# Optimization experiments

Hardware: AMD Instinct MI355X
Metric: run time of the kernel (lower is better)

The kernel has to match this reference:

```python
import jax, jax.numpy as jnp
import numpy as np

B, T, G, M, D = 8, 2048, 2, 1024, 256
ALPHA = -1.0      # config['dist_to_logits_alpha']
TAU = 2.0         # curr_temp = max_temp at init
EPS = 1e-10


def setup_inputs() -> dict:
    key = jax.random.key(0)
    k1, k2, k3 = jax.random.split(key, 3)
    x = jax.random.normal(k1, (B, T, G * D), dtype=jnp.float32)
    # nn.init.uniform_(embedding, -0.999, 0.999)
    embedding = jax.random.uniform(k2, (G, M, D), dtype=jnp.float32, minval=-0.999, maxval=0.999)
    # uniform noise for gumbel sampling, clipped away from {0,1}
    gumbel_u = jax.random.uniform(k3, (B * T, G, M), dtype=jnp.float32, minval=1e-6, maxval=1.0 - 1e-6)
    return {"x": x, "embedding": embedding, "gumbel_u": gumbel_u}


def reference(x, embedding, gumbel_u):
    b, t, c = x.shape
    g, m, d = embedding.shape
    xf = x.reshape(-1, g, d)                                  # [N, G, D]

    sq_e = jnp.sum(embedding ** 2, axis=-1)                   # [G, M]
    sq_x = jnp.sum(xf ** 2, axis=-1, keepdims=True)           # [N, G, 1]
    cross = jnp.einsum('ngd,gmd->ngm', xf, embedding)         # [N, G, M]
    logits = ALPHA * (sq_e[None] + sq_x - 2.0 * cross)        # [N, G, M]

    # hard-assignment code perplexity
    hard_x = jax.nn.one_hot(jnp.argmax(logits, axis=-1), m, dtype=logits.dtype)
    hard_probs = hard_x.mean(axis=0)                          # [G, M]
    code_perplexity = -jnp.sum(hard_probs * jnp.log2(hard_probs + EPS), axis=-1)

    # soft-assignment prob perplexity
    avg_probs = jax.nn.softmax(logits, axis=-1).mean(axis=0)  # [G, M]
    prob_perplexity = -jnp.sum(avg_probs * jnp.log2(avg_probs + EPS), axis=-1)

    # gumbel-softmax (hard=True, straight-through)
    gumbels = -jnp.log(-jnp.log(gumbel_u))
    y_soft = jax.nn.softmax((logits + gumbels) / TAU, axis=-1)
    idx = jnp.argmax(y_soft, axis=-1)                         # [N, G]
    y_hard = jax.nn.one_hot(idx, m, dtype=y_soft.dtype)
    st = y_hard + y_soft - jax.lax.stop_gradient(y_soft)      # straight-through one-hot

    # weighted sum over the codebook (avoids [N, G, M, D] blowup of the original)
    quantized = jnp.einsum('ngm,gmd->ngd', st, embedding).reshape(b, t, c)

    quantization_inds = idx.reshape(b, t, g).astype(jnp.int32)
    # use_vq_loss=True: F.mse_loss(x, quantized.detach())
    commitment_loss = jnp.mean((x - jax.lax.stop_gradient(quantized)) ** 2)

    return quantized, code_perplexity, prob_perplexity, quantization_inds, commitment_loss
```

## Files before the change

### kernel.cpp

```cpp
#include <hip/hip_runtime.h>
#include <math.h>

#define NTOT 16384
#define GG 2
#define MM 1024
#define DD 256

#define OFF_Q  ((size_t)0)
#define OFF_CP ((size_t)8388608)
#define OFF_PP ((size_t)8388610)
#define OFF_I  ((size_t)8388612)
#define OFF_L  ((size_t)8421380)

#define SHIFT 40.0f
#define REFINE_GAP 0.03f

typedef __attribute__((ext_vector_type(8))) short bf16x8;
typedef __attribute__((ext_vector_type(4))) float f32x4;
typedef unsigned short u16;
typedef unsigned int u32;

__device__ inline float wave_sum_f(float v) {
#pragma unroll
  for (int o = 32; o > 0; o >>= 1) v += __shfl_xor(v, o);
  return v;
}
__device__ inline u16 f2bf(float f) {
  u32 u = __float_as_uint(f);
  return (u16)((u + 0x7fffu + ((u >> 16) & 1u)) >> 16);
}
__device__ inline float bf2f(u16 h) {
  return __uint_as_float(((u32)h) << 16);
}
__device__ inline void async16(const void* g, void* l) {
  __builtin_amdgcn_global_load_lds(
      (const __attribute__((address_space(1))) u32*)g,
      (__attribute__((address_space(3))) u32*)l, 16, 0, 0);
}

#define WS_INVZ   32768
#define WS_EHSW   163840
#define WS_ELSW   1212416
#define WS_EST    2260992
#define WS_NEED3  (2260992ull + 2ull * MM * (size_t)NTOT * GG)

__global__ void vq_init2(const float* __restrict__ emb, float* __restrict__ sq_e,
                         float* __restrict__ avg, int* __restrict__ hist,
                         double* __restrict__ loss, u16* __restrict__ eh,
                         u16* __restrict__ el, int do_split) {
  const int row = blockIdx.x * 4 + (threadIdx.x >> 6);
  const int lane = threadIdx.x & 63;
  float4 e4 = *(const float4*)&emb[(size_t)row * DD + lane * 4];
  float s = e4.x * e4.x + e4.y * e4.y + e4.z * e4.z + e4.w * e4.w;
  s = wave_sum_f(s);
  if (do_split) {
    ushort4 h, l;
    h.x = f2bf(e4.x); l.x = f2bf(e4.x - bf2f(h.x));
    h.y = f2bf(e4.y); l.y = f2bf(e4.y - bf2f(h.y));
    h.z = f2bf(e4.z); l.z = f2bf(e4.z - bf2f(h.z));
    h.w = f2bf(e4.w); l.w = f2bf(e4.w - bf2f(h.w));
    *(ushort4*)&eh[(size_t)row * DD + lane * 4] = h;
    *(ushort4*)&el[(size_t)row * DD + lane * 4] = l;
  }
  if (lane == 0) sq_e[row] = s;
  if (blockIdx.x == 0) {
    for (int i = threadIdx.x; i < GG * MM; i += 256) { avg[i] = 0.f; hist[i] = 0; }
    if (threadIdx.x == 0) *loss = 0.0;
  }
}

__global__ void vq_init_swz(const float* __restrict__ emb, u16* __restrict__ eh_sw,
                            u16* __restrict__ el_sw) {
  int tid = blockIdx.x * 256 + threadIdx.x;
  int g = tid >> 15, rem = tid & 32767;
  int col = rem >> 5, kc = rem & 31;
  const float* src = emb + ((size_t)(g * MM + col)) * DD + kc * 8;
  float4 fa = *(const float4*)src;
  float4 fb = *(const float4*)(src + 4);
  float f[8] = {fa.x, fa.y, fa.z, fa.w, fb.x, fb.y, fb.z, fb.w};
  u16 hi[8], lo[8];
#pragma unroll
  for (int j = 0; j < 8; ++j) {
    hi[j] = f2bf(f[j]);
    lo[j] = f2bf(f[j] - bf2f(hi[j]));
  }
  int ct = col >> 6, cg = (col >> 4) & 3, l15 = col & 15;
  int ks = kc >> 2, quad = kc & 3;
  size_t chunk = ((((size_t)g * 16 + ct) * 8 + ks) * 4 + cg) * 64 + quad * 16 + l15;
  ushort4* dh = (ushort4*)(eh_sw + chunk * 8);
  ushort4* dl = (ushort4*)(el_sw + chunk * 8);
  dh[0] = make_ushort4(hi[0], hi[1], hi[2], hi[3]);
  dh[1] = make_ushort4(hi[4], hi[5], hi[6], hi[7]);
  dl[0] = make_ushort4(lo[0], lo[1], lo[2], lo[3]);
  dl[1] = make_ushort4(lo[4], lo[5], lo[6], lo[7]);
}

__global__ __launch_bounds__(256, 2) void vq_main3(
    const float* __restrict__ x, const float* __restrict__ emb,
    const float* __restrict__ gum, const float* __restrict__ sq_e,
    const u16* __restrict__ eh_sw, const u16* __restrict__ el_sw,
    float* __restrict__ out, u16* __restrict__ est, float* __restrict__ invZ_ws,
    int* __restrict__ hist, double* __restrict__ loss) {
  __shared__ u16 bt[2][32768];
  __shared__ int fidx_lds[128];

  const int g = blockIdx.y;
  const int n0 = blockIdx.x * 128;
  const int t = threadIdx.x;
  const int wave = t >> 6, lane = t & 63;
  const int quad = lane >> 4, l15 = lane & 15;
  const int nw = n0 + wave * 32;

  float* xs = (float*)&bt[0][0];
  {
    const float* xb = x + (size_t)nw * (GG * DD) + (size_t)g * DD;
#pragma unroll 4
    for (int j = 0; j < 32; ++j) {
      float4 v = *(const float4*)(xb + (size_t)j * (GG * DD) + lane * 4);
      *(float4*)&xs[wave * 8192 + j * 256 + ((lane ^ (j & 7)) << 2)] = v;
    }
  }
  __syncthreads();

  bf16x8 ah[2][8], al[2][8];
#pragma unroll
  for (int s = 0; s < 2; ++s) {
#pragma unroll
    for (int ks = 0; ks < 8; ++ks) {
      int row = s * 16 + l15;
      int c0 = ks * 8 + quad * 2;
      const float* base = &xs[wave * 8192 + row * 256];
      float4 f0 = *(const float4*)&base[((c0 ^ (row & 7)) << 2)];
      float4 f1 = *(const float4*)&base[(((c0 + 1) ^ (row & 7)) << 2)];
      float f[8] = {f0.x, f0.y, f0.z, f0.w, f1.x, f1.y, f1.z, f1.w};
#pragma unroll
      for (int j = 0; j < 8; ++j) {
        u16 h = f2bf(f[j]);
        ah[s][ks][j] = (short)h;
        al[s][ks][j] = (short)f2bf(f[j] - bf2f(h));
      }
    }
  }
  __syncthreads();

  const u16* sgh = eh_sw + (size_t)g * 16 * 16384;
  const u16* sgl = el_sw + (size_t)g * 16 * 16384;

  auto stage = [&](int ct, int buf) {
    const u16* sh = sgh + (size_t)ct * 16384;
    const u16* sl = sgl + (size_t)ct * 16384;
    u16* dh = &bt[buf][0];
    u16* dl = &bt[buf][16384];
#pragma unroll
    for (int j = 0; j < 8; ++j) {
      int slot = j * 4 + wave;
      async16(sh + slot * 512 + lane * 8, dh + slot * 512);
      async16(sl + slot * 512 + lane * 8, dl + slot * 512);
    }
  };

  float Zl[8], hv[8], z1[8], z2[8];
  int hid[8], i1[8], i2[8];
#pragma unroll
  for (int i = 0; i < 8; ++i) {
    Zl[i] = 0.f; hv[i] = -INFINITY; z1[i] = -INFINITY; z2[i] = -INFINITY;
    hid[i] = 0; i1[i] = 0; i2[i] = 0;
  }

  stage(0, 0);

#pragma unroll 1
  for (int ct = 0; ct < 16; ++ct) {
    __syncthreads();
    if (ct < 15) stage(ct + 1, (ct + 1) & 1);
    const u16* bh_p = &bt[ct & 1][0];
    const u16* bl_p = &bt[ct & 1][16384];
#pragma unroll 1
    for (int cg = 0; cg < 4; ++cg) {
      const int colG = ct * 64 + cg * 16 + l15;
      float sqv = sq_e[g * MM + colG];
      float gv[8];
#pragma unroll
      for (int s = 0; s < 2; ++s)
#pragma unroll
        for (int r = 0; r < 4; ++r)
          gv[s * 4 + r] =
              gum[((size_t)(nw + s * 16 + quad * 4 + r) * GG + g) * MM + colG];

      f32x4 c00 = {0,0,0,0}, c01 = {0,0,0,0}, c02 = {0,0,0,0};
      f32x4 c10 = {0,0,0,0}, c11 = {0,0,0,0}, c12 = {0,0,0,0};
#pragma unroll
      for (int ks = 0; ks < 8; ++ks) {
        int off = ((ks * 4 + cg) * 64 + lane) * 8;
        bf16x8 bh = *(const bf16x8*)(bh_p + off);
        bf16x8 bl = *(const bf16x8*)(bl_p + off);
        c00 = __builtin_amdgcn_mfma_f32_16x16x32_bf16(ah[0][ks], bh, c00, 0, 0, 0);
        c01 = __builtin_amdgcn_mfma_f32_16x16x32_bf16(ah[0][ks], bl, c01, 0, 0, 0);
        c02 = __builtin_amdgcn_mfma_f32_16x16x32_bf16(al[0][ks], bh, c02, 0, 0, 0);
        c10 = __builtin_amdgcn_mfma_f32_16x16x32_bf16(ah[1][ks], bh, c10, 0, 0, 0);
        c11 = __builtin_amdgcn_mfma_f32_16x16x32_bf16(ah[1][ks], bl, c11, 0, 0, 0);
        c12 = __builtin_amdgcn_mfma_f32_16x16x32_bf16(al[1][ks], bh, c12, 0, 0, 0);
      }
#pragma unroll
      for (int s = 0; s < 2; ++s) {
        const f32x4& a0 = s ? c10 : c00;
        const f32x4& a1 = s ? c11 : c01;
        const f32x4& a2 = s ? c12 : c02;
        ushort4 pk;
        u16* pp = (u16*)&pk;
#pragma unroll
        for (int r = 0; r < 4; ++r) {
          float lp = 2.f * (a0[r] + a1[r] + a2[r]) - sqv + SHIFT;
          float ev = expf(fminf(lp, 80.f));
          Zl[s * 4 + r] += ev;
          pp[r] = f2bf(ev);
          if (lp > hv[s * 4 + r]) { hv[s * 4 + r] = lp; hid[s * 4 + r] = colG; }
          float zz = lp - logf(-logf(gv[s * 4 + r]));
          if (zz > z1[s * 4 + r]) {
            z2[s * 4 + r] = z1[s * 4 + r]; i2[s * 4 + r] = i1[s * 4 + r];
            z1[s * 4 + r] = zz; i1[s * 4 + r] = colG;
          } else if (zz > z2[s * 4 + r]) {
            z2[s * 4 + r] = zz; i2[s * 4 + r] = colG;
          }
        }
        *(ushort4*)&est[((size_t)(g * MM + colG) << 14) + nw + s * 16 + quad * 4] = pk;
      }
    }
  }

#pragma unroll 1
  for (int s = 0; s < 2; ++s) {
#pragma unroll 1
    for (int r = 0; r < 4; ++r) {
      const int idx = s * 4 + r;
      const int row = wave * 32 + s * 16 + quad * 4 + r;
      const int n = n0 + row;
      float Zr = Zl[idx], hvr = hv[idx];
      int hir = hid[idx];
      float v1 = z1[idx], v2 = z2[idx];
      int j1 = i1[idx], j2 = i2[idx];
#pragma unroll
      for (int o = 1; o <= 8; o <<= 1) {
        Zr += __shfl_xor(Zr, o);
        float ohv = __shfl_xor(hvr, o); int ohi = __shfl_xor(hir, o);
        if (ohv > hvr || (ohv == hvr && ohi < hir)) { hvr = ohv; hir = ohi; }
        float w1 = __shfl_xor(v1, o), w2 = __shfl_xor(v2, o);
        int k1 = __shfl_xor(j1, o), k2 = __shfl_xor(j2, o);
        if (w1 > v1 || (w1 == v1 && k1 < j1)) {
          if (v1 > w2 || (v1 == w2 && j1 < k2)) { v2 = v1; j2 = j1; }
          else { v2 = w2; j2 = k2; }
          v1 = w1; j1 = k1;
        } else if (w1 > v2 || (w1 == v2 && k1 < j2)) { v2 = w1; j2 = k1; }
      }
      int fidx = j1;
      if (v1 - v2 < REFINE_GAP) {
        const float* xrow = x + (size_t)n * (GG * DD) + (size_t)g * DD;
        const float* eA = emb + ((size_t)g * MM + j1) * DD;
        const float* eB = emb + ((size_t)g * MM + j2) * DD;
        double dA = 0, sA = 0, dB = 0, sB = 0;
#pragma unroll
        for (int k = 0; k < 16; ++k) {
          int d = l15 * 16 + k;
          double xv = (double)xrow[d];
          double ea = (double)eA[d], eb = (double)eB[d];
          dA += xv * ea; sA += ea * ea;
          dB += xv * eb; sB += eb * eb;
        }
#pragma unroll
        for (int o = 1; o <= 8; o <<= 1) {
          dA += __shfl_xor(dA, o); sA += __shfl_xor(sA, o);
          dB += __shfl_xor(dB, o); sB += __shfl_xor(sB, o);
        }
        double uA = (double)gum[((size_t)n * GG + g) * MM + j1];
        double uB = (double)gum[((size_t)n * GG + g) * MM + j2];
        double zA = 2.0 * dA - sA - log(-log(uA));
        double zB = 2.0 * dB - sB - log(-log(uB));
        if (zB > zA || (zB == zA && j2 < j1)) fidx = j2;
      }
      if (l15 == 0) {
        out[OFF_I + (size_t)n * GG + g] = (float)fidx;
        atomicAdd(&hist[g * MM + hir], 1);
        invZ_ws[g * NTOT + n] = 1.f / Zr;
        fidx_lds[row] = fidx;
      }
    }
  }
  __syncthreads();

  {
    float ls = 0.f;
#pragma unroll 4
    for (int j = 0; j < 32; ++j) {
      int idx = j * 256 + t;
      int row = idx >> 6, f4 = idx & 63;
      int n = n0 + row, fi = fidx_lds[row];
      float4 e4 = *(const float4*)&emb[((size_t)g * MM + fi) * DD + f4 * 4];
      float4 x4 = *(const float4*)&x[(size_t)n * (GG * DD) + (size_t)g * DD + f4 * 4];
      *(float4*)&out[OFF_Q + (size_t)n * (GG * DD) + (size_t)g * DD + f4 * 4] = e4;
      float dx = x4.x - e4.x, dy = x4.y - e4.y, dz = x4.z - e4.z, dw = x4.w - e4.w;
      ls += dx * dx + dy * dy + dz * dz + dw * dw;
    }
    ls = wave_sum_f(ls);
    if (lane == 0) atomicAdd(loss, (double)ls);
  }
}

__global__ void vq_avg(const u16* __restrict__ est, const float* __restrict__ invZ,
                       float* __restrict__ avg) {
  int wid = blockIdx.x * 4 + (threadIdx.x >> 6);
  int lane = threadIdx.x & 63;
  const u16* base = est + ((size_t)wid << 14);
  const float* zp = invZ + ((wid >> 10) << 14);
  float acc = 0.f;
#pragma unroll 4
  for (int it = 0; it < 64; ++it) {
    int n = it * 256 + lane * 4;
    ushort4 e4 = *(const ushort4*)(base + n);
    float4 z4 = *(const float4*)(zp + n);
    acc += bf2f(e4.x) * z4.x + bf2f(e4.y) * z4.y +
           bf2f(e4.z) * z4.z + bf2f(e4.w) * z4.w;
  }
  acc = wave_sum_f(acc);
  if (lane == 0) avg[wid] = acc;
}

__global__ void vq_fin(const float* __restrict__ avg, const int* __restrict__ hist,
                       const double* __restrict__ loss, float* __restrict__ out) {
  int g = blockIdx.x, t = threadIdx.x;
  float cp = 0.f, pp = 0.f;
  for (int m = t; m < MM; m += 256) {
    float hp = (float)hist[g * MM + m] * (1.f / 16384.f);
    cp += hp * log2f(hp + 1e-10f);
    float ap = avg[g * MM + m] * (1.f / 16384.f);
    pp += ap * log2f(ap + 1e-10f);
  }
  cp = wave_sum_f(cp);
  pp = wave_sum_f(pp);
  __shared__ float sc[4], sp[4];
  int wave = t >> 6, lane = t & 63;
  if (lane == 0) { sc[wave] = cp; sp[wave] = pp; }
  __syncthreads();
  if (t == 0) {
    out[OFF_CP + g] = -(sc[0] + sc[1] + sc[2] + sc[3]);
    out[OFF_PP + g] = -(sp[0] + sp[1] + sp[2] + sp[3]);
    if (g == 0) out[OFF_L] = (float)(*loss * (1.0 / 8388608.0));
  }
}

__global__ __launch_bounds__(256, 3) void vq_main_fast(
    const float* __restrict__ x, const float* __restrict__ emb,
    const float* __restrict__ gum, const float* __restrict__ sq_e,
    const u16* __restrict__ eh, const u16* __restrict__ el,
    float* __restrict__ out, float* __restrict__ avg,
    int* __restrict__ hist, double* __restrict__ loss) {
  __shared__ u16 est_lds[4][16][264];
  __shared__ float colsum[MM];
  __shared__ float red[16][4][8];
  __shared__ float fin_invZ[16];
  __shared__ int fin_idx[16];

  const int g = blockIdx.y;
  const int n0 = blockIdx.x * 16;
  const int t = threadIdx.x;
  const int wave = t >> 6, lane = t & 63;
  const int quad = lane >> 4, l15 = lane & 15;
  const int wm0 = wave * 256;

  for (int i = t; i < MM; i += 256) colsum[i] = 0.f;

  bf16x8 ah[8], al[8];
  {
    const float* xr = x + (size_t)(n0 + l15) * (GG * DD) + (size_t)g * DD + quad * 8;
#pragma unroll
    for (int ks = 0; ks < 8; ++ks) {
      float4 fa = *(const float4*)(xr + ks * 32);
      float4 fb = *(const float4*)(xr + ks * 32 + 4);
      float f[8] = {fa.x, fa.y, fa.z, fa.w, fb.x, fb.y, fb.z, fb.w};
#pragma unroll
      for (int j = 0; j < 8; ++j) {
        u16 h = f2bf(f[j]);
        ah[ks][j] = (short)h;
        al[ks][j] = (short)f2bf(f[j] - bf2f(h));
      }
    }
  }
  const u16* ehb = eh + ((size_t)g * MM + wm0 + l15) * DD + quad * 8;
  const u16* elb = el + ((size_t)g * MM + wm0 + l15) * DD + quad * 8;
  const float* sqb = sq_e + g * MM + wm0 + l15;

  float Z[4] = {0.f, 0.f, 0.f, 0.f};
  float hv[4] = {-INFINITY, -INFINITY, -INFINITY, -INFINITY};
  int hid[4] = {0, 0, 0, 0};
  float z1[4] = {-INFINITY, -INFINITY, -INFINITY, -INFINITY};
  float z2[4] = {-INFINITY, -INFINITY, -INFINITY, -INFINITY};
  int i1[4] = {0, 0, 0, 0}, i2[4] = {0, 0, 0, 0};

#pragma unroll 2
  for (int tt = 0; tt < 16; ++tt) {
    float sqv = sqb[tt * 16];
    float gv[4];
#pragma unroll
    for (int r = 0; r < 4; ++r)
      gv[r] = gum[((size_t)(n0 + quad * 4 + r) * GG + g) * MM + wm0 + tt * 16 + l15];
    f32x4 a0 = {0,0,0,0}, a1 = {0,0,0,0}, a2 = {0,0,0,0};
#pragma unroll
    for (int ks = 0; ks < 8; ++ks) {
      bf16x8 bh = *(const bf16x8*)(ehb + (size_t)tt * 16 * DD + ks * 32);
      bf16x8 bl = *(const bf16x8*)(elb + (size_t)tt * 16 * DD + ks * 32);
      a0 = __builtin_amdgcn_mfma_f32_16x16x32_bf16(ah[ks], bh, a0, 0, 0, 0);
      a1 = __builtin_amdgcn_mfma_f32_16x16x32_bf16(ah[ks], bl, a1, 0, 0, 0);
      a2 = __builtin_amdgcn_mfma_f32_16x16x32_bf16(al[ks], bh, a2, 0, 0, 0);
    }
    const int colL = tt * 16 + l15;
    const int colG = wm0 + colL;
#pragma unroll
    for (int r = 0; r < 4; ++r) {
      float lp = 2.f * (a0[r] + a1[r] + a2[r]) - sqv + SHIFT;
      float ev = expf(fminf(lp, 80.f));
      Z[r] += ev;
      est_lds[wave][quad * 4 + r][colL] = f2bf(ev);
      if (lp > hv[r]) { hv[r] = lp; hid[r] = colG; }
      float zz = lp - logf(-logf(gv[r]));
      if (zz > z1[r]) { z2[r] = z1[r]; i2[r] = i1[r]; z1[r] = zz; i1[r] = colG; }
      else if (zz > z2[r]) { z2[r] = zz; i2[r] = colG; }
    }
  }
#pragma unroll
  for (int r = 0; r < 4; ++r) {
    float Zr = Z[r], hvr = hv[r];
    int hir = hid[r];
    float v1 = z1[r], v2 = z2[r];
    int j1 = i1[r], j2 = i2[r];
#pragma unroll
    for (int o = 1; o <= 8; o <<= 1) {
      Zr += __shfl_xor(Zr, o);
      float ohv = __shfl_xor(hvr, o); int ohi = __shfl_xor(hir, o);
      if (ohv > hvr || (ohv == hvr && ohi < hir)) { hvr = ohv; hir = ohi; }
      float w1 = __shfl_xor(v1, o), w2 = __shfl_xor(v2, o);
      int k1 = __shfl_xor(j1, o), k2 = __shfl_xor(j2, o);
      if (w1 > v1 || (w1 == v1 && k1 < j1)) {
        if (v1 > w2 || (v1 == w2 && j1 < k2)) { v2 = v1; j2 = j1; }
        else { v2 = w2; j2 = k2; }
        v1 = w1; j1 = k1;
      } else if (w1 > v2 || (w1 == v2 && k1 < j2)) { v2 = w1; j2 = k1; }
    }
    if (l15 == 0) {
      float* rp = red[quad * 4 + r][wave];
      rp[0] = Zr; rp[1] = hvr; rp[2] = __int_as_float(hir);
      rp[3] = v1; rp[4] = __int_as_float(j1);
      rp[5] = v2; rp[6] = __int_as_float(j2);
    }
  }
  __syncthreads();
  if (t < 16) {
    const int row = t, n = n0 + row;
    float Zf = 0.f, hvf = -INFINITY; int hif = 0;
    float v1 = -INFINITY, v2 = -INFINITY; int j1 = 0, j2 = 0;
    for (int w = 0; w < 4; ++w) {
      const float* rp = red[row][w];
      Zf += rp[0];
      float ohv = rp[1]; int ohi = __float_as_int(rp[2]);
      if (ohv > hvf || (ohv == hvf && ohi < hif)) { hvf = ohv; hif = ohi; }
      float w1 = rp[3], w2 = rp[5];
      int k1 = __float_as_int(rp[4]), k2 = __float_as_int(rp[6]);
      if (w1 > v1 || (w1 == v1 && k1 < j1)) {
        if (v1 > w2 || (v1 == w2 && j1 < k2)) { v2 = v1; j2 = j1; }
        else { v2 = w2; j2 = k2; }
        v1 = w1; j1 = k1;
      } else if (w1 > v2 || (w1 == v2 && k1 < j2)) { v2 = w1; j2 = k1; }
    }
    int fidx = j1;
    if (v1 - v2 < REFINE_GAP) {
      const float* xrow = x + (size_t)n * (GG * DD) + (size_t)g * DD;
      const float* eA = emb + ((size_t)g * MM + j1) * DD;
      const float* eB = emb + ((size_t)g * MM + j2) * DD;
      double dA = 0, sA = 0, dB = 0, sB = 0;
      for (int d = 0; d < DD; ++d) {
        double xv = xrow[d], ea = eA[d], eb = eB[d];
        dA += xv * ea; sA += ea * ea;
        dB += xv * eb; sB += eb * eb;
      }
      double uA = gum[((size_t)n * GG + g) * MM + j1];
      double uB = gum[((size_t)n * GG + g) * MM + j2];
      double zA = 2.0 * dA - sA - log(-log(uA));
      double zB = 2.0 * dB - sB - log(-log(uB));
      if (zB > zA || (zB == zA && j2 < j1)) fidx = j2;
    }
    out[OFF_I + (size_t)n * GG + g] = (float)fidx;
    atomicAdd(&hist[g * MM + hif], 1);
    fin_invZ[row] = 1.f / Zf;
    fin_idx[row] = fidx;
  }
  __syncthreads();
  {
    const int row = t >> 4, c = (t & 15) * 16;
    const int n = n0 + row, fidx = fin_idx[row];
    const float* er = emb + ((size_t)g * MM + fidx) * DD + c;
    const float* xq = x + (size_t)n * (GG * DD) + (size_t)g * DD + c;
    float* op = out + OFF_Q + (size_t)n * (GG * DD) + (size_t)g * DD + c;
    float ls = 0.f;
#pragma unroll
    for (int j = 0; j < 4; ++j) {
      float4 e4 = *(const float4*)(er + j * 4);
      float4 x4 = *(const float4*)(xq + j * 4);
      *(float4*)(op + j * 4) = e4;
      float dx = x4.x - e4.x, dy = x4.y - e4.y, dz = x4.z - e4.z, dw = x4.w - e4.w;
      ls += dx * dx + dy * dy + dz * dz + dw * dw;
    }
    ls = wave_sum_f(ls);
    if (lane == 0) atomicAdd(loss, (double)ls);
  }
  float iZ[4];
#pragma unroll
  for (int r = 0; r < 4; ++r) iZ[r] = fin_invZ[quad * 4 + r];
#pragma unroll 1
  for (int tt = 0; tt < 16; ++tt) {
    float v = 0.f;
#pragma unroll
    for (int r = 0; r < 4; ++r)
      v += bf2f(est_lds[wave][quad * 4 + r][tt * 16 + l15]) * iZ[r];
    v += __shfl_xor(v, 16);
    v += __shfl_xor(v, 32);
    if (lane < 16) colsum[wm0 + tt * 16 + lane] += v;
  }
  __syncthreads();
  for (int i = t; i < MM; i += 256) atomicAdd(&avg[g * MM + i], colsum[i]);
}

extern "C" void kernel_launch(void* const* d_in, const int* in_sizes, int n_in,
                              void* d_out, int out_size, void* d_ws, size_t ws_size,
                              hipStream_t stream) {
  const float* x = (const float*)d_in[0];
  const float* emb = (const float*)d_in[1];
  const float* gum = (const float*)d_in[2];
  float* out = (float*)d_out;

  float* sq_e = (float*)d_ws;
  float* avg = (float*)((char*)d_ws + 8192);
  int* hist = (int*)((char*)d_ws + 16384);
  double* loss = (double*)((char*)d_ws + 24576);

  if (ws_size >= WS_NEED3) {
    float* invZ = (float*)((char*)d_ws + WS_INVZ);
    u16* eh_sw = (u16*)((char*)d_ws + WS_EHSW);
    u16* el_sw = (u16*)((char*)d_ws + WS_ELSW);
    u16* est = (u16*)((char*)d_ws + WS_EST);
    vq_init2<<<512, 256, 0, stream>>>(emb, sq_e, avg, hist, loss, eh_sw, el_sw, 0);
    vq_init_swz<<<256, 256, 0, stream>>>(emb, eh_sw, el_sw);
    vq_main3<<<dim3(NTOT / 128, GG), 256, 0, stream>>>(
        x, emb, gum, sq_e, eh_sw, el_sw, out, est, invZ, hist, loss);
    vq_avg<<<512, 256, 0, stream>>>(est, invZ, avg);
    vq_fin<<<GG, 256, 0, stream>>>(avg, hist, loss, out);
  } else {
    u16* eh = (u16*)((char*)d_ws + 32768);
    u16* el = eh + (size_t)GG * MM * DD;
    vq_init2<<<512, 256, 0, stream>>>(emb, sq_e, avg, hist, loss, eh, el, 1);
    vq_main_fast<<<dim3(NTOT / 16, GG), 256, 0, stream>>>(
        x, emb, gum, sq_e, eh, el, out, avg, hist, loss);
    vq_fin<<<GG, 256, 0, stream>>>(avg, hist, loss, out);
  }
}
```

Measured before the change: 400.5 us.

## Split 128-row tile across 8 waves with 16 rows each instead of 4x32

```diff
diff --git a/kernel.cpp b/kernel.cpp
--- a/kernel.cpp
+++ b/kernel.cpp
@@ -95,7 +95,7 @@
   dl[1] = make_ushort4(lo[4], lo[5], lo[6], lo[7]);
 }
 
-__global__ __launch_bounds__(256, 2) void vq_main3(
+__global__ __launch_bounds__(512, 2) void vq_main3(
     const float* __restrict__ x, const float* __restrict__ emb,
     const float* __restrict__ gum, const float* __restrict__ sq_e,
     const u16* __restrict__ eh_sw, const u16* __restrict__ el_sw,
@@ -109,36 +109,32 @@
   const int t = threadIdx.x;
   const int wave = t >> 6, lane = t & 63;
   const int quad = lane >> 4, l15 = lane & 15;
-  const int nw = n0 + wave * 32;
+  const int nw = n0 + wave * 16;
 
   float* xs = (float*)&bt[0][0];
   {
     const float* xb = x + (size_t)nw * (GG * DD) + (size_t)g * DD;
 #pragma unroll 4
-    for (int j = 0; j < 32; ++j) {
+    for (int j = 0; j < 16; ++j) {
       float4 v = *(const float4*)(xb + (size_t)j * (GG * DD) + lane * 4);
-      *(float4*)&xs[wave * 8192 + j * 256 + ((lane ^ (j & 7)) << 2)] = v;
-    }
-  }
-  __syncthreads();
-
-  bf16x8 ah[2][8], al[2][8];
-#pragma unroll
-  for (int s = 0; s < 2; ++s) {
-#pragma unroll
-    for (int ks = 0; ks < 8; ++ks) {
-      int row = s * 16 + l15;
-      int c0 = ks * 8 + quad * 2;
-      const float* base = &xs[wave * 8192 + row * 256];
-      float4 f0 = *(const float4*)&base[((c0 ^ (row & 7)) << 2)];
-      float4 f1 = *(const float4*)&base[(((c0 + 1) ^ (row & 7)) << 2)];
-      float f[8] = {f0.x, f0.y, f0.z, f0.w, f1.x, f1.y, f1.z, f1.w};
-#pragma unroll
-      for (int j = 0; j < 8; ++j) {
-        u16 h = f2bf(f[j]);
-        ah[s][ks][j] = (short)h;
-        al[s][ks][j] = (short)f2bf(f[j] - bf2f(h));
-      }
+      *(float4*)&xs[wave * 4096 + j * 256 + ((lane ^ (j & 7)) << 2)] = v;
+    }
+  }
+
+  bf16x8 ah[8], al[8];
+#pragma unroll
+  for (int ks = 0; ks < 8; ++ks) {
+    int row = l15;
+    int c0 = ks * 8 + quad * 2;
+    const float* base = &xs[wave * 4096 + row * 256];
+    float4 f0 = *(const float4*)&base[((c0 ^ (row & 7)) << 2)];
+    float4 f1 = *(const float4*)&base[(((c0 + 1) ^ (row & 7)) << 2)];
+    float f[8] = {f0.x, f0.y, f0.z, f0.w, f1.x, f1.y, f1.z, f1.w};
+#pragma unroll
+    for (int j = 0; j < 8; ++j) {
+      u16 h = f2bf(f[j]);
+      ah[ks][j] = (short)h;
+      al[ks][j] = (short)f2bf(f[j] - bf2f(h));
     }
   }
   __syncthreads();
@@ -152,17 +148,17 @@
     u16* dh = &bt[buf][0];
     u16* dl = &bt[buf][16384];
 #pragma unroll
-    for (int j = 0; j < 8; ++j) {
-      int slot = j * 4 + wave;
+    for (int j = 0; j < 4; ++j) {
+      int slot = j * 8 + wave;
       async16(sh + slot * 512 + lane * 8, dh + slot * 512);
       async16(sl + slot * 512 + lane * 8, dl + slot * 512);
     }
   };
 
-  float Zl[8], hv[8], z1[8], z2[8];
-  int hid[8], i1[8], i2[8];
-#pragma unroll
-  for (int i = 0; i < 8; ++i) {
+  float Zl[4], hv[4], z1[4], z2[4];
+  int hid[4], i1[4], i2[4];
+#pragma unroll
+  for (int i = 0; i < 4; ++i) {
     Zl[i] = 0.f; hv[i] = -INFINITY; z1[i] = -INFINITY; z2[i] = -INFINITY;
     hid[i] = 0; i1[i] = 0; i2[i] = 0;
   }
@@ -179,110 +175,93 @@
     for (int cg = 0; cg < 4; ++cg) {
       const int colG = ct * 64 + cg * 16 + l15;
       float sqv = sq_e[g * MM + colG];
-      float gv[8];
-#pragma unroll
-      for (int s = 0; s < 2; ++s)
-#pragma unroll
-        for (int r = 0; r < 4; ++r)
-          gv[s * 4 + r] =
-              gum[((size_t)(nw + s * 16 + quad * 4 + r) * GG + g) * MM + colG];
-
-      f32x4 c00 = {0,0,0,0}, c01 = {0,0,0,0}, c02 = {0,0,0,0};
-      f32x4 c10 = {0,0,0,0}, c11 = {0,0,0,0}, c12 = {0,0,0,0};
+      float gv[4];
+#pragma unroll
+      for (int r = 0; r < 4; ++r)
+        gv[r] = gum[((size_t)(nw + quad * 4 + r) * GG + g) * MM + colG];
+
+      f32x4 c0 = {0,0,0,0}, c1 = {0,0,0,0}, c2 = {0,0,0,0};
 #pragma unroll
       for (int ks = 0; ks < 8; ++ks) {
         int off = ((ks * 4 + cg) * 64 + lane) * 8;
         bf16x8 bh = *(const bf16x8*)(bh_p + off);
         bf16x8 bl = *(const bf16x8*)(bl_p + off);
-        c00 = __builtin_amdgcn_mfma_f32_16x16x32_bf16(ah[0][ks], bh, c00, 0, 0, 0);
-        c01 = __builtin_amdgcn_mfma_f32_16x16x32_bf16(ah[0][ks], bl, c01, 0, 0, 0);
-        c02 = __builtin_amdgcn_mfma_f32_16x16x32_bf16(al[0][ks], bh, c02, 0, 0, 0);
-        c10 = __builtin_amdgcn_mfma_f32_16x16x32_bf16(ah[1][ks], bh, c10, 0, 0, 0);
-        c11 = __builtin_amdgcn_mfma_f32_16x16x32_bf16(ah[1][ks], bl, c11, 0, 0, 0);
-        c12 = __builtin_amdgcn_mfma_f32_16x16x32_bf16(al[1][ks], bh, c12, 0, 0, 0);
+        c0 = __builtin_amdgcn_mfma_f32_16x16x32_bf16(ah[ks], bh, c0, 0, 0, 0);
+        c1 = __builtin_amdgcn_mfma_f32_16x16x32_bf16(ah[ks], bl, c1, 0, 0, 0);
+        c2 = __builtin_amdgcn_mfma_f32_16x16x32_bf16(al[ks], bh, c2, 0, 0, 0);
       }
-#pragma unroll
-      for (int s = 0; s < 2; ++s) {
-        const f32x4& a0 = s ? c10 : c00;
-        const f32x4& a1 = s ? c11 : c01;
-        const f32x4& a2 = s ? c12 : c02;
-        ushort4 pk;
-        u16* pp = (u16*)&pk;
-#pragma unroll
-        for (int r = 0; r < 4; ++r) {
-          float lp = 2.f * (a0[r] + a1[r] + a2[r]) - sqv + SHIFT;
-          float ev = expf(fminf(lp, 80.f));
-          Zl[s * 4 + r] += ev;
-          pp[r] = f2bf(ev);
-          if (lp > hv[s * 4 + r]) { hv[s * 4 + r] = lp; hid[s * 4 + r] = colG; }
-          float zz = lp - logf(-logf(gv[s * 4 + r]));
-          if (zz > z1[s * 4 + r]) {
-            z2[s * 4 + r] = z1[s * 4 + r]; i2[s * 4 + r] = i1[s * 4 + r];
-            z1[s * 4 + r] = zz; i1[s * 4 + r] = colG;
-          } else if (zz > z2[s * 4 + r]) {
-            z2[s * 4 + r] = zz; i2[s * 4 + r] = colG;
-          }
+      ushort4 pk;
+      u16* pp = (u16*)&pk;
+#pragma unroll
+      for (int r = 0; r < 4; ++r) {
+        float lp = 2.f * (c0[r] + c1[r] + c2[r]) - sqv + SHIFT;
+        float ev = expf(fminf(lp, 80.f));
+        Zl[r] += ev;
+        pp[r] = f2bf(ev);
+        if (lp > hv[r]) { hv[r] = lp; hid[r] = colG; }
+        float zz = lp - logf(-logf(gv[r]));
+        if (zz > z1[r]) {
+          z2[r] = z1[r]; i2[r] = i1[r];
+          z1[r] = zz; i1[r] = colG;
+        } else if (zz > z2[r]) {
+          z2[r] = zz; i2[r] = colG;
         }
-        *(ushort4*)&est[((size_t)(g * MM + colG) << 14) + nw + s * 16 + quad * 4] = pk;
       }
+      *(ushort4*)&est[((size_t)(g * MM + colG) << 14) + nw + quad * 4] = pk;
     }
   }
 
 #pragma unroll 1
-  for (int s = 0; s < 2; ++s) {
-#pragma unroll 1
-    for (int r = 0; r < 4; ++r) {
-      const int idx = s * 4 + r;
-      const int row = wave * 32 + s * 16 + quad * 4 + r;
-      const int n = n0 + row;
-      float Zr = Zl[idx], hvr = hv[idx];
-      int hir = hid[idx];
-      float v1 = z1[idx], v2 = z2[idx];
-      int j1 = i1[idx], j2 = i2[idx];
+  for (int r = 0; r < 4; ++r) {
+    const int row = wave * 16 + quad * 4 + r;
+    const int n = n0 + row;
+    float Zr = Zl[r], hvr = hv[r];
+    int hir = hid[r];
+    float v1 = z1[r], v2 = z2[r];
+    int j1 = i1[r], j2 = i2[r];
+#pragma unroll
+    for (int o = 1; o <= 8; o <<= 1) {
+      Zr += __shfl_xor(Zr, o);
+      float ohv = __shfl_xor(hvr, o); int ohi = __shfl_xor(hir, o);
+      if (ohv > hvr || (ohv == hvr && ohi < hir)) { hvr = ohv; hir = ohi; }
+      float w1 = __shfl_xor(v1, o), w2 = __shfl_xor(v2, o);
+      int k1 = __shfl_xor(j1, o), k2 = __shfl_xor(j2, o);
+      if (w1 > v1 || (w1 == v1 && k1 < j1)) {
+        if (v1 > w2 || (v1 == w2 && j1 < k2)) { v2 = v1; j2 = j1; }
+        else { v2 = w2; j2 = k2; }
+        v1 = w1; j1 = k1;
+      } else if (w1 > v2 || (w1 == v2 && k1 < j2)) { v2 = w1; j2 = k1; }
+    }
+    int fidx = j1;
+    if (v1 - v2 < REFINE_GAP) {
+      const float* xrow = x + (size_t)n * (GG * DD) + (size_t)g * DD;
+      const float* eA = emb + ((size_t)g * MM + j1) * DD;
+      const float* eB = emb + ((size_t)g * MM + j2) * DD;
+      double dA = 0, sA = 0, dB = 0, sB = 0;
+#pragma unroll
+      for (int k = 0; k < 16; ++k) {
+        int d = l15 * 16 + k;
+        double xv = (double)xrow[d];
+        double ea = (double)eA[d], eb = (double)eB[d];
+        dA += xv * ea; sA += ea * ea;
+        dB += xv * eb; sB += eb * eb;
+      }
 #pragma unroll
       for (int o = 1; o <= 8; o <<= 1) {
-        Zr += __shfl_xor(Zr, o);
-        float ohv = __shfl_xor(hvr, o); int ohi = __shfl_xor(hir, o);
-        if (ohv > hvr || (ohv == hvr && ohi < hir)) { hvr = ohv; hir = ohi; }
-        float w1 = __shfl_xor(v1, o), w2 = __shfl_xor(v2, o);
-        int k1 = __shfl_xor(j1, o), k2 = __shfl_xor(j2, o);
-        if (w1 > v1 || (w1 == v1 && k1 < j1)) {
-          if (v1 > w2 || (v1 == w2 && j1 < k2)) { v2 = v1; j2 = j1; }
-          else { v2 = w2; j2 = k2; }
-          v1 = w1; j1 = k1;
-        } else if (w1 > v2 || (w1 == v2 && k1 < j2)) { v2 = w1; j2 = k1; }
+        dA += __shfl_xor(dA, o); sA += __shfl_xor(sA, o);
+        dB += __shfl_xor(dB, o); sB += __shfl_xor(sB, o);
       }
-      int fidx = j1;
-      if (v1 - v2 < REFINE_GAP) {
-        const float* xrow = x + (size_t)n * (GG * DD) + (size_t)g * DD;
-        const float* eA = emb + ((size_t)g * MM + j1) * DD;
-        const float* eB = emb + ((size_t)g * MM + j2) * DD;
-        double dA = 0, sA = 0, dB = 0, sB = 0;
-#pragma unroll
-        for (int k = 0; k < 16; ++k) {
-          int d = l15 * 16 + k;
-          double xv = (double)xrow[d];
-          double ea = (double)eA[d], eb = (double)eB[d];
-          dA += xv * ea; sA += ea * ea;
-          dB += xv * eb; sB += eb * eb;
-        }
-#pragma unroll
-        for (int o = 1; o <= 8; o <<= 1) {
-          dA += __shfl_xor(dA, o); sA += __shfl_xor(sA, o);
-          dB += __shfl_xor(dB, o); sB += __shfl_xor(sB, o);
-        }
-        double uA = (double)gum[((size_t)n * GG + g) * MM + j1];
-        double uB = (double)gum[((size_t)n * GG + g) * MM + j2];
-        double zA = 2.0 * dA - sA - log(-log(uA));
-        double zB = 2.0 * dB - sB - log(-log(uB));
-        if (zB > zA || (zB == zA && j2 < j1)) fidx = j2;
-      }
-      if (l15 == 0) {
-        out[OFF_I + (size_t)n * GG + g] = (float)fidx;
-        atomicAdd(&hist[g * MM + hir], 1);
-        invZ_ws[g * NTOT + n] = 1.f / Zr;
-        fidx_lds[row] = fidx;
-      }
+      double uA = (double)gum[((size_t)n * GG + g) * MM + j1];
+      double uB = (double)gum[((size_t)n * GG + g) * MM + j2];
+      double zA = 2.0 * dA - sA - log(-log(uA));
+      double zB = 2.0 * dB - sB - log(-log(uB));
+      if (zB > zA || (zB == zA && j2 < j1)) fidx = j2;
+    }
+    if (l15 == 0) {
+      out[OFF_I + (size_t)n * GG + g] = (float)fidx;
+      atomicAdd(&hist[g * MM + hir], 1);
+      invZ_ws[g * NTOT + n] = 1.f / Zr;
+      fidx_lds[row] = fidx;
     }
   }
   __syncthreads();
@@ -290,8 +269,8 @@
   {
     float ls = 0.f;
 #pragma unroll 4
-    for (int j = 0; j < 32; ++j) {
-      int idx = j * 256 + t;
+    for (int j = 0; j < 16; ++j) {
+      int idx = j * 512 + t;
       int row = idx >> 6, f4 = idx & 63;
       int n = n0 + row, fi = fidx_lds[row];
       float4 e4 = *(const float4*)&emb[((size_t)g * MM + fi) * DD + f4 * 4];
@@ -547,7 +526,7 @@
     u16* est = (u16*)((char*)d_ws + WS_EST);
     vq_init2<<<512, 256, 0, stream>>>(emb, sq_e, avg, hist, loss, eh_sw, el_sw, 0);
     vq_init_swz<<<256, 256, 0, stream>>>(emb, eh_sw, el_sw);
-    vq_main3<<<dim3(NTOT / 128, GG), 256, 0, stream>>>(
+    vq_main3<<<dim3(NTOT / 128, GG), 512, 0, stream>>>(
         x, emb, gum, sq_e, eh_sw, el_sw, out, est, invZ, hist, loss);
     vq_avg<<<512, 256, 0, stream>>>(est, invZ, avg);
     vq_fin<<<GG, 256, 0, stream>>>(avg, hist, loss, out);
```

Measured after the change: 364.3 us. -9.1%, faster.
